# Optimization experiments

Hardware: AMD Instinct MI355X
Metric: run time of the kernel (lower is better)

## Reference

```python
import jax, jax.numpy as jnp
import numpy as np

N_NODES = 12800
N_EDGES = 204800
DIM = 16
EDGE_DIM = 4
NUM_FEAT = 3


def setup_inputs() -> dict:
    key = jax.random.key(0)
    ks = jax.random.split(key, 16)
    s = 0.1
    return {
        "x": jax.random.normal(ks[0], (N_NODES, NUM_FEAT), jnp.float32),
        "edge_index": jax.random.randint(ks[1], (2, N_EDGES), 0, N_NODES, jnp.int32),
        "edge_attr": jax.random.uniform(ks[2], (N_EDGES, EDGE_DIM), jnp.float32),
        "lin0_w": jax.random.normal(ks[3], (DIM, NUM_FEAT), jnp.float32) * s,
        "lin0_b": jax.random.normal(ks[4], (DIM,), jnp.float32) * s,
        "nn1_w": jax.random.normal(ks[5], (DIM, EDGE_DIM), jnp.float32) * s,
        "nn1_b": jax.random.normal(ks[6], (DIM,), jnp.float32) * s,
        "nn2_w": jax.random.normal(ks[7], (DIM * DIM, DIM), jnp.float32) * s,
        "nn2_b": jax.random.normal(ks[8], (DIM * DIM,), jnp.float32) * s,
        "conv_root": jax.random.normal(ks[9], (DIM, DIM), jnp.float32) * s,
        "conv_bias": jax.random.normal(ks[10], (DIM,), jnp.float32) * s,
        "gru_w_ih": jax.random.normal(ks[11], (3 * DIM, DIM), jnp.float32) * s,
        "gru_w_hh": jax.random.normal(ks[12], (3 * DIM, DIM), jnp.float32) * s,
        "gru_b_ih": jax.random.normal(ks[13], (3 * DIM,), jnp.float32) * s,
        "gru_b_hh": jax.random.normal(ks[14], (3 * DIM,), jnp.float32) * s,
    }


def _forward(x, edge_index, edge_attr, lin0_w, lin0_b, nn1_w, nn1_b, nn2_w, nn2_b,
             conv_root, conv_bias, gru_w_ih, gru_w_hh, gru_b_ih, gru_b_hh):
    n = x.shape[0]
    dim = lin0_w.shape[0]
    src, dst = edge_index[0], edge_index[1]

    # edge-conditioned weight matrices, shared across the 6 rounds: [E, dim, dim]
    e_hidden = jax.nn.relu(edge_attr @ nn1_w.T + nn1_b)
    edge_w = (e_hidden @ nn2_w.T + nn2_b).reshape(-1, dim, dim)

    # in-degree for mean aggregation (0 -> divide by 1, result stays 0)
    deg = jax.ops.segment_sum(jnp.ones_like(dst, dtype=x.dtype), dst, num_segments=n)
    inv_deg = (1.0 / jnp.maximum(deg, 1.0))[:, None]

    out = jax.nn.relu(x @ lin0_w.T + lin0_b)  # [N, dim]
    h = out
    for _ in range(6):
        # gather -> per-edge matmul -> scatter-mean
        msg = jnp.einsum('ed,edk->ek', out[src], edge_w)  # [E, dim]
        aggr = jax.ops.segment_sum(msg, dst, num_segments=n) * inv_deg
        m = jax.nn.relu(aggr + out @ conv_root + conv_bias)
        # single GRU step (seq_len = 1)
        gi = m @ gru_w_ih.T + gru_b_ih  # [N, 3*dim]
        gh = h @ gru_w_hh.T + gru_b_hh
        i_r, i_z, i_n = jnp.split(gi, 3, axis=-1)
        h_r, h_z, h_n = jnp.split(gh, 3, axis=-1)
        r = jax.nn.sigmoid(i_r + h_r)
        z = jax.nn.sigmoid(i_z + h_z)
        nhat = jnp.tanh(i_n + r * h_n)
        h = (1.0 - z) * nhat + z * h
        out = h
    return out


def reference(x, edge_index, edge_attr, lin0_w, lin0_b, nn1_w, nn1_b, nn2_w, nn2_b,
              conv_root, conv_bias, gru_w_ih, gru_w_hh, gru_b_ih, gru_b_hh):
    return _forward(x, edge_index, edge_attr, lin0_w, lin0_b, nn1_w, nn1_b, nn2_w,
                    nn2_b, conv_root, conv_bias, gru_w_ih, gru_w_hh, gru_b_ih, gru_b_hh)
```

## Files before the change

### kernel.cpp

```cpp
#include <hip/hip_runtime.h>

#define NN 12800
#define NE 204800
#define BCAP 64
#define NPB 50
#define RTHR (NPB * 16)

#define OFF_W2 0
#define OFF_CR 4416
#define OFF_WI 4736
#define OFF_WH 5696
#define OFF_CB 6656
#define OFF_BI 6672
#define OFF_BH 6720
#define PACKN  6768

__device__ __align__(16) float g_outA[NN * 16];
__device__ __align__(16) float g_outB[NN * 16];
__device__ __align__(16) float g_ehsB[NN * BCAP * 16];
__device__ __align__(16) int g_srcB[NN * BCAP];
__device__ int g_cnt[NN];
__device__ __align__(16) float g_wpack[PACKN];

__global__ __launch_bounds__(256) void k_setup(const int* __restrict__ ei,
                                               const float* __restrict__ x,
                                               const float* __restrict__ lw,
                                               const float* __restrict__ lb,
                                               const float* __restrict__ attr,
                                               const float* __restrict__ w1,
                                               const float* __restrict__ b1,
                                               const float* __restrict__ nn2_w,
                                               const float* __restrict__ nn2_b,
                                               const float* __restrict__ cr,
                                               const float* __restrict__ cb,
                                               const float* __restrict__ wi,
                                               const float* __restrict__ wh,
                                               const float* __restrict__ bi,
                                               const float* __restrict__ bh) {
    int gid = blockIdx.x * 256 + threadIdx.x;

    if (blockIdx.x == 0) {
        int tt = threadIdx.x;
        for (int i = tt; i < 4096; i += 256)
            g_wpack[OFF_W2 + (i & 15) * 276 + ((i >> 4) & 15) * 16 + (i >> 8)] = nn2_w[i];
        g_wpack[OFF_W2 + (tt >> 4) * 276 + 256 + (tt & 15)] = nn2_b[tt];
        g_wpack[OFF_CR + (tt & 15) * 20 + (tt >> 4)] = cr[tt];
        for (int i = tt; i < 768; i += 256) {
            g_wpack[OFF_WI + (i >> 4) * 20 + (i & 15)] = wi[i];
            g_wpack[OFF_WH + (i >> 4) * 20 + (i & 15)] = wh[i];
        }
        if (tt < 16) g_wpack[OFF_CB + tt] = cb[tt];
        if (tt < 48) { g_wpack[OFF_BI + tt] = bi[tt]; g_wpack[OFF_BH + tt] = bh[tt]; }
    }

    if (gid < NN) {
        int n = gid;
        float x0 = x[n * 3 + 0], x1 = x[n * 3 + 1], x2 = x[n * 3 + 2];
        float v[16];
#pragma unroll
        for (int j = 0; j < 16; ++j) {
            float t = lb[j] + x0 * lw[j * 3 + 0] + x1 * lw[j * 3 + 1] + x2 * lw[j * 3 + 2];
            v[j] = fmaxf(t, 0.0f);
        }
#pragma unroll
        for (int j = 0; j < 16; j += 4)
            *(float4*)(g_outA + n * 16 + j) = make_float4(v[j], v[j + 1], v[j + 2], v[j + 3]);
    }

    int e = gid;
    int s = ei[e], d = ei[NE + e];
    float4 a = *(const float4*)(attr + e * 4);
    float v[16];
#pragma unroll
    for (int j = 0; j < 16; ++j) {
        float t = b1[j] + a.x * w1[j * 4 + 0] + a.y * w1[j * 4 + 1] +
                  a.z * w1[j * 4 + 2] + a.w * w1[j * 4 + 3];
        v[j] = fmaxf(t, 0.0f);
    }
    int pos = atomicAdd(&g_cnt[d], 1);
    if (pos < BCAP) {
        int slot = d * BCAP + pos;
        g_srcB[slot] = s;
#pragma unroll
        for (int j = 0; j < 16; j += 4)
            *(float4*)(g_ehsB + slot * 16 + j) = make_float4(v[j], v[j + 1], v[j + 2], v[j + 3]);
    }
}

__global__ __launch_bounds__(RTHR) void k_round(float* __restrict__ out_final,
                                                int flip, int last) {
    __shared__ __align__(16) float s_pack[PACKN];
    int t = threadIdx.x;
    {
        const float4* srcp = (const float4*)g_wpack;
        float4* dstp = (float4*)s_pack;
        for (int idx = t; idx < PACKN / 4; idx += RTHR) dstp[idx] = srcp[idx];
    }
    __syncthreads();

    const float* s_W2  = s_pack + OFF_W2;
    const float* s_crT = s_pack + OFF_CR;
    const float* s_wi  = s_pack + OFF_WI;
    const float* s_wh  = s_pack + OFF_WH;
    const float* s_cb  = s_pack + OFF_CB;
    const float* s_bi  = s_pack + OFF_BI;
    const float* s_bh  = s_pack + OFF_BH;

    const float* cur = flip ? g_outB : g_outA;
    float*       nxt = flip ? g_outA : g_outB;

    const int grp = t >> 4, j = t & 15;
    const int n = blockIdx.x * NPB + grp;
    int deg = min(g_cnt[n], BCAP);
    if (last && j == 0) g_cnt[n] = 0;
    const int base = n * BCAP;

    float Gd[16];
#pragma unroll
    for (int d = 0; d < 16; ++d) Gd[d] = 0.0f;
    float r16 = 0.0f;
#pragma unroll 4
    for (int q = 0; q < deg; ++q) {
        int slot = base + q;
        int s = min(g_srcB[slot], NN - 1);
        const float* orow = cur + s * 16;
        float ej = g_ehsB[slot * 16 + j];
        float4 o0 = *(const float4*)(orow + 0);
        float4 o1 = *(const float4*)(orow + 4);
        float4 o2 = *(const float4*)(orow + 8);
        float4 o3 = *(const float4*)(orow + 12);
        Gd[0]  += ej * o0.x; Gd[1]  += ej * o0.y; Gd[2]  += ej * o0.z; Gd[3]  += ej * o0.w;
        Gd[4]  += ej * o1.x; Gd[5]  += ej * o1.y; Gd[6]  += ej * o1.z; Gd[7]  += ej * o1.w;
        Gd[8]  += ej * o2.x; Gd[9]  += ej * o2.y; Gd[10] += ej * o2.z; Gd[11] += ej * o2.w;
        Gd[12] += ej * o3.x; Gd[13] += ej * o3.y; Gd[14] += ej * o3.z; Gd[15] += ej * o3.w;
        r16 += orow[j];
    }

    const float* wj = s_W2 + j * 276;
    float part[16];
#pragma unroll
    for (int kp = 0; kp < 16; ++kp) {
        const float* w = wj + kp * 16;
        float4 w0 = *(const float4*)(w + 0);
        float4 w1 = *(const float4*)(w + 4);
        float4 w2 = *(const float4*)(w + 8);
        float4 w3 = *(const float4*)(w + 12);
        part[kp] = Gd[0] * w0.x + Gd[1] * w0.y + Gd[2] * w0.z + Gd[3] * w0.w
                 + Gd[4] * w1.x + Gd[5] * w1.y + Gd[6] * w1.z + Gd[7] * w1.w
                 + Gd[8] * w2.x + Gd[9] * w2.y + Gd[10] * w2.z + Gd[11] * w2.w
                 + Gd[12] * w3.x + Gd[13] * w3.y + Gd[14] * w3.z + Gd[15] * w3.w;
    }
    {
        float4 b0 = *(const float4*)(wj + 256);
        float4 b1 = *(const float4*)(wj + 260);
        float4 b2v = *(const float4*)(wj + 264);
        float4 b3 = *(const float4*)(wj + 268);
        part[0] += r16 * b0.x;  part[1] += r16 * b0.y;  part[2] += r16 * b0.z;  part[3] += r16 * b0.w;
        part[4] += r16 * b1.x;  part[5] += r16 * b1.y;  part[6] += r16 * b1.z;  part[7] += r16 * b1.w;
        part[8] += r16 * b2v.x; part[9] += r16 * b2v.y; part[10] += r16 * b2v.z; part[11] += r16 * b2v.w;
        part[12] += r16 * b3.x; part[13] += r16 * b3.y; part[14] += r16 * b3.z; part[15] += r16 * b3.w;
    }

    float w8[8];
#pragma unroll
    for (int i = 0; i < 8; ++i) {
        int keep = 2 * i + (j & 1);
        w8[i] = part[keep] + __shfl_xor(part[keep ^ 1], 1);
    }
    float w4[4];
#pragma unroll
    for (int i = 0; i < 4; ++i) {
        int keep = 2 * i + ((j >> 1) & 1);
        w4[i] = w8[keep] + __shfl_xor(w8[keep ^ 1], 2);
    }
    float w2[2];
#pragma unroll
    for (int i = 0; i < 2; ++i) {
        int keep = 2 * i + ((j >> 2) & 1);
        w2[i] = w4[keep] + __shfl_xor(w4[keep ^ 1], 4);
    }
    float aggr;
    {
        int keep = (j >> 3) & 1;
        aggr = w2[keep] + __shfl_xor(w2[keep ^ 1], 8);
    }
    float invd = 1.0f / (float)(deg > 0 ? deg : 1);
    float a_k = aggr * invd;
    const int k = j;

    const float* nrow = cur + n * 16;
    float4 q0 = *(const float4*)(nrow + 0);
    float4 q1 = *(const float4*)(nrow + 4);
    float4 q2 = *(const float4*)(nrow + 8);
    float4 q3 = *(const float4*)(nrow + 12);
    float o[16] = {q0.x, q0.y, q0.z, q0.w, q1.x, q1.y, q1.z, q1.w,
                   q2.x, q2.y, q2.z, q2.w, q3.x, q3.y, q3.z, q3.w};
    float ok = o[k];

    float mcc = s_cb[k] + a_k;
    {
        const float* c = s_crT + k * 20;
        float4 c0 = *(const float4*)(c + 0);
        float4 c1 = *(const float4*)(c + 4);
        float4 c2 = *(const float4*)(c + 8);
        float4 c3 = *(const float4*)(c + 12);
        mcc += o[0] * c0.x + o[1] * c0.y + o[2] * c0.z + o[3] * c0.w
             + o[4] * c1.x + o[5] * c1.y + o[6] * c1.z + o[7] * c1.w
             + o[8] * c2.x + o[9] * c2.y + o[10] * c2.z + o[11] * c2.w
             + o[12] * c3.x + o[13] * c3.y + o[14] * c3.z + o[15] * c3.w;
    }
    float m = fmaxf(mcc, 0.0f);

    float md[16];
#pragma unroll
    for (int d = 0; d < 16; ++d) md[d] = __shfl(m, d, 16);

    float ir = s_bi[k], iz = s_bi[16 + k], in_ = s_bi[32 + k];
    float hr = s_bh[k], hz = s_bh[16 + k], hh = s_bh[32 + k];
#pragma unroll
    for (int g = 0; g < 3; ++g) {
        const float* wrow_i = s_wi + (g * 16 + k) * 20;
        const float* wrow_h = s_wh + (g * 16 + k) * 20;
        float acc_i = 0.0f, acc_h = 0.0f;
#pragma unroll
        for (int d4 = 0; d4 < 4; ++d4) {
            float4 wiv = *(const float4*)(wrow_i + d4 * 4);
            float4 whv = *(const float4*)(wrow_h + d4 * 4);
            acc_i += md[d4 * 4] * wiv.x + md[d4 * 4 + 1] * wiv.y
                   + md[d4 * 4 + 2] * wiv.z + md[d4 * 4 + 3] * wiv.w;
            acc_h += o[d4 * 4] * whv.x + o[d4 * 4 + 1] * whv.y
                   + o[d4 * 4 + 2] * whv.z + o[d4 * 4 + 3] * whv.w;
        }
        if (g == 0) { ir += acc_i; hr += acc_h; }
        else if (g == 1) { iz += acc_i; hz += acc_h; }
        else { in_ += acc_i; hh += acc_h; }
    }
    float rg = 1.0f / (1.0f + __expf(-(ir + hr)));
    float z  = 1.0f / (1.0f + __expf(-(iz + hz)));
    float nh = tanhf(in_ + rg * hh);
    float hnew = (1.0f - z) * nh + z * ok;

    if (last) out_final[n * 16 + k] = hnew;
    else      nxt[n * 16 + k] = hnew;
}

extern "C" void kernel_launch(void* const* d_in, const int* in_sizes, int n_in,
                              void* d_out, int out_size, void* d_ws, size_t ws_size,
                              hipStream_t stream) {
    const float* x         = (const float*)d_in[0];
    const int*   ei        = (const int*)d_in[1];
    const float* edge_attr = (const float*)d_in[2];
    const float* lin0_w    = (const float*)d_in[3];
    const float* lin0_b    = (const float*)d_in[4];
    const float* nn1_w     = (const float*)d_in[5];
    const float* nn1_b     = (const float*)d_in[6];
    const float* nn2_w     = (const float*)d_in[7];
    const float* nn2_b     = (const float*)d_in[8];
    const float* conv_root = (const float*)d_in[9];
    const float* conv_bias = (const float*)d_in[10];
    const float* gru_w_ih  = (const float*)d_in[11];
    const float* gru_w_hh  = (const float*)d_in[12];
    const float* gru_b_ih  = (const float*)d_in[13];
    const float* gru_b_hh  = (const float*)d_in[14];
    float* out = (float*)d_out;

    k_setup<<<NE / 256, 256, 0, stream>>>(ei, x, lin0_w, lin0_b, edge_attr,
                                          nn1_w, nn1_b, nn2_w, nn2_b, conv_root,
                                          conv_bias, gru_w_ih, gru_w_hh,
                                          gru_b_ih, gru_b_hh);

    for (int r = 0; r < 6; ++r) {
        k_round<<<NN / NPB, RTHR, 0, stream>>>(out, r & 1, r == 5 ? 1 : 0);
    }
}
```

Before: 236.4 us.

## Sort nodes by in-degree to balance per-wavefront work in round kernel

Adds a single-block kernel that histograms node in-degrees, prefix-sums them with a wavefront scan, and writes a permutation that assigns nodes to blocks and 16-lane groups so that groups sharing a wavefront have similar degree. Degree classes are dealt round-robin across all blocks so each block gets a similar mix of work. Each round kernel then reads its node index through this permutation. This targets loop divergence within wavefronts (four 16-lane groups share a 64-wide wavefront and run to the largest degree) and imbalance across blocks. The cost is an extra serial launch and one indirect load per thread, and it scatters output writes across node order.

```diff
diff --git a/kernel.cpp b/kernel.cpp
--- a/kernel.cpp
+++ b/kernel.cpp
@@ -20,6 +20,7 @@
 __device__ __align__(16) float g_ehsB[NN * BCAP * 16];
 __device__ __align__(16) int g_srcB[NN * BCAP];
 __device__ int g_cnt[NN];
+__device__ int g_perm[NN];
 __device__ __align__(16) float g_wpack[PACKN];
 
 __global__ __launch_bounds__(256) void k_setup(const int* __restrict__ ei,
@@ -87,6 +88,41 @@
     }
 }
 
+__global__ __launch_bounds__(1024) void k_perm() {
+    __shared__ int hist[64];
+    int t = threadIdx.x;
+    if (t < 64) hist[t] = 0;
+    __syncthreads();
+    for (int n = t; n < NN; n += 1024)
+        atomicAdd(&hist[min(g_cnt[n], 63)], 1);
+    __syncthreads();
+    if (t < 64) {
+        int v = hist[t];
+        int incl = v;
+#pragma unroll
+        for (int off = 1; off < 64; off <<= 1) {
+            int u = __shfl_up(incl, off, 64);
+            if (t >= off) incl += u;
+        }
+        hist[t] = incl - v;
+    }
+    __syncthreads();
+    for (int n = t; n < NN; n += 1024) {
+        int s = atomicAdd(&hist[min(g_cnt[n], 63)], 1);
+        int blk, grp;
+        if (s < 12288) {
+            int c = s >> 2, r = s & 3;
+            blk = c & 255;
+            grp = ((c >> 8) << 2) + r;
+        } else {
+            int l = s - 12288;
+            blk = l & 255;
+            grp = 48 + (l >> 8);
+        }
+        g_perm[blk * NPB + grp] = n;
+    }
+}
+
 __global__ __launch_bounds__(RTHR) void k_round(float* __restrict__ out_final,
                                                 int flip, int last) {
     __shared__ __align__(16) float s_pack[PACKN];
@@ -110,7 +146,7 @@
     float*       nxt = flip ? g_outA : g_outB;
 
     const int grp = t >> 4, j = t & 15;
-    const int n = blockIdx.x * NPB + grp;
+    const int n = min(max(g_perm[blockIdx.x * NPB + grp], 0), NN - 1);
     int deg = min(g_cnt[n], BCAP);
     if (last && j == 0) g_cnt[n] = 0;
     const int base = n * BCAP;
@@ -268,6 +304,7 @@
                                           nn1_w, nn1_b, nn2_w, nn2_b, conv_root,
                                           conv_bias, gru_w_ih, gru_w_hh,
                                           gru_b_ih, gru_b_hh);
+    k_perm<<<1, 1024, 0, stream>>>();
 
     for (int r = 0; r < 6; ++r) {
         k_round<<<NN / NPB, RTHR, 0, stream>>>(out, r & 1, r == 5 ? 1 : 0);
```

After: 235.5 us. About the same (-0.4%).
